# Kernel optimization log

Hardware: AMD Instinct MI355X
Metric: run time of the kernel (lower is better)

Reference implementation:

```python
import jax, jax.numpy as jnp
import numpy as np

N, D_IN, D_OUT, N_CTRS, K = 16384, 64, 64, 512, 16


def setup_inputs() -> dict:
    key = jax.random.key(0)
    k1, k2, k3, k4 = jax.random.split(key, 4)
    x = jax.random.normal(k1, (N, D_IN), dtype=jnp.float32)
    ctrs = jax.random.normal(k2, (N_CTRS, D_IN), dtype=jnp.float32)
    Wv = jax.random.normal(k3, (N_CTRS, D_IN, D_OUT), dtype=jnp.float32) * 0.02
    Ov = jax.random.normal(k4, (N_CTRS, D_OUT), dtype=jnp.float32) * 0.02
    return {"x": x, "ctrs": ctrs, "Wv": Wv, "Ov": Ov, "k": K}


def reference(x, ctrs, Wv, Ov, k):
    n = x.shape[0]
    # squared distances via expansion (same math as sum((x-c)^2), avoids [n,C,d] blowup)
    x2 = jnp.sum(x * x, axis=1, keepdims=True)            # [n,1]
    c2 = jnp.sum(ctrs * ctrs, axis=1)                     # [C]
    dist_sq = x2 + c2[None, :] - 2.0 * (x @ ctrs.T)       # [n,C]
    # k nearest centers; softmax over negative squared distances of the k selected
    neg_top, idx = jax.lax.top_k(-dist_sq, k)             # [n,k] each
    scores = jax.nn.softmax(neg_top, axis=1)              # [n,k]
    # dense soft-assignment matrix (only k nonzeros per row), as in the torch code
    A = jnp.zeros_like(dist_sq).at[jnp.arange(n)[:, None], idx].set(scores)  # [n,C]
    # per-token affine mix: sum_c A[n,c] * (x[n] @ Wv[c] + Ov[c])
    scored_weights = jnp.einsum('nc,cgp->ngp', A, Wv)     # [n,d_in,d_out]
    out = jnp.einsum('ngp,ng->np', scored_weights, x) + A @ Ov  # [n,d_out]
    return out
```

## Files before the change

### kernel.cpp

```cpp
#include <hip/hip_runtime.h>

#define N_TOK 16384
#define D 64
#define NC 512
#define KSEL 16
#define NPAIR (N_TOK * KSEL)
#define PADCAP 327168

typedef __attribute__((ext_vector_type(8))) short short8;
typedef __attribute__((ext_vector_type(16))) float float16;

__device__ __forceinline__ unsigned fkey(float f) {
    unsigned u = __float_as_uint(f);
    return (u & 0x80000000u) ? ~u : (u | 0x80000000u);
}
__device__ __forceinline__ float funkey(unsigned k) {
    unsigned u = (k & 0x80000000u) ? (k & 0x7fffffffu) : ~k;
    return __uint_as_float(u);
}
__device__ __forceinline__ unsigned short bfr(float f) {
    unsigned u = __float_as_uint(f);
    return (unsigned short)((u + 0x7FFFu + ((u >> 16) & 1u)) >> 16);
}

__device__ __forceinline__ void ins16(unsigned (&run)[16], unsigned k) {
    #pragma unroll
    for (int r = 0; r < 16; ++r) {
        unsigned mx = run[r] > k ? run[r] : k;
        unsigned mn = run[r] > k ? k : run[r];
        run[r] = mx; k = mn;
    }
}

__global__ __launch_bounds__(256) void topk12_kernel(
    const float* __restrict__ x, const float* __restrict__ ctrs,
    unsigned* __restrict__ pk) {
    __shared__ __align__(16) unsigned char pool[65536];
    float* xsT = (float*)pool;
    float* csT = (float*)(pool + 32768);
    unsigned* Sbk = (unsigned*)pool;
    unsigned* mbp = (unsigned*)pool;

    const int t = threadIdx.x;
    const int tb = blockIdx.x >> 2;
    const int p = blockIdx.x & 3;
    const int base = tb * 128;
    const int cbase = p * 128;

    #pragma unroll
    for (int i = 0; i < 8; ++i) {
        int e = t + 256 * i;
        int r = e >> 4, j = e & 15;
        int col = 64 * ((r >> 2) & 1) + 4 * (r >> 3) + (r & 3);
        float4 v = *(const float4*)(x + (base + r) * D + 4 * j);
        xsT[(4 * j + 0) * 128 + col] = v.x;
        xsT[(4 * j + 1) * 128 + col] = v.y;
        xsT[(4 * j + 2) * 128 + col] = v.z;
        xsT[(4 * j + 3) * 128 + col] = v.w;
    }
    #pragma unroll
    for (int i = 0; i < 8; ++i) {
        int e = t + 256 * i;
        int r = e >> 4, j = e & 15;
        int col = 64 * ((r >> 2) & 1) + 4 * (r >> 3) + (r & 3);
        float4 v = *(const float4*)(ctrs + (cbase + r) * D + 4 * j);
        csT[(4 * j + 0) * 128 + col] = v.x;
        csT[(4 * j + 1) * 128 + col] = v.y;
        csT[(4 * j + 2) * 128 + col] = v.z;
        csT[(4 * j + 3) * 128 + col] = v.w;
    }
    __syncthreads();

    const int tg = t >> 4;
    const int cg = t & 15;

    float acc[8][8];
    float acc2[8];
    #pragma unroll
    for (int i = 0; i < 8; ++i) {
        acc2[i] = 0.f;
        #pragma unroll
        for (int j = 0; j < 8; ++j) acc[i][j] = 0.f;
    }

    #pragma unroll 2
    for (int k = 0; k < 64; ++k) {
        const float* xr = xsT + k * 128;
        const float* cr = csT + k * 128;
        float4 xa0 = *(const float4*)(xr + 4 * tg);
        float4 xa1 = *(const float4*)(xr + 64 + 4 * tg);
        float4 cb0 = *(const float4*)(cr + 4 * cg);
        float4 cb1 = *(const float4*)(cr + 64 + 4 * cg);
        float xv[8] = {xa0.x, xa0.y, xa0.z, xa0.w, xa1.x, xa1.y, xa1.z, xa1.w};
        float cv[8] = {cb0.x, cb0.y, cb0.z, cb0.w, cb1.x, cb1.y, cb1.z, cb1.w};
        #pragma unroll
        for (int i = 0; i < 8; ++i) {
            #pragma unroll
            for (int j = 0; j < 8; ++j)
                acc[i][j] = fmaf(xv[i], cv[j], acc[i][j]);
        }
        #pragma unroll
        for (int j = 0; j < 8; ++j) acc2[j] = fmaf(cv[j], cv[j], acc2[j]);
    }
    __syncthreads();

    #pragma unroll
    for (int s = 0; s < 16; ++s) {
        const int i = s >> 1;
        const int jv = s & 1;
        unsigned kq[4];
        #pragma unroll
        for (int q = 0; q < 4; ++q) {
            int j = 4 * jv + q;
            float sq = fmaf(2.f, acc[i][j], -acc2[j]);
            kq[q] = (fkey(sq) & 0xFFFFFE00u) | (unsigned)(cbase + 8 * cg + j);
        }
        *(uint4*)(Sbk + (8 * tg + i) * 128 + 8 * cg + 4 * jv) =
            make_uint4(kq[0], kq[1], kq[2], kq[3]);
    }
    __syncthreads();

    const int tok = t & 127;
    const int h = t >> 7;
    unsigned run[16];
    #pragma unroll
    for (int r = 0; r < 16; ++r) run[r] = 0u;
    #pragma unroll
    for (int s = 0; s < 16; ++s) {
        int cq = h * 16 + ((s + tok) & 15);
        uint4 kv = *(const uint4*)(Sbk + tok * 128 + 4 * cq);
        ins16(run, kv.x); ins16(run, kv.y); ins16(run, kv.z); ins16(run, kv.w);
    }
    __syncthreads();

    #pragma unroll
    for (int r = 0; r < 16; ++r) mbp[tok * 33 + h * 16 + r] = run[r];
    __syncthreads();

    if (t < 128) {
        const unsigned* A = mbp + t * 33;
        const unsigned* B = A + 16;
        unsigned m[16];
        int ia = 0, ib = 0;
        unsigned va = A[0], vb = B[0];
        #pragma unroll
        for (int r = 0; r < 16; ++r) {
            bool ta = va > vb;
            m[r] = ta ? va : vb;
            if (ta) { ++ia; va = (ia < 16) ? A[ia] : 0u; }
            else    { ++ib; vb = (ib < 16) ? B[ib] : 0u; }
        }
        uint4* dst = (uint4*)(pk + (size_t)(base + t) * 64 + p * 16);
        dst[0] = make_uint4(m[0], m[1], m[2], m[3]);
        dst[1] = make_uint4(m[4], m[5], m[6], m[7]);
        dst[2] = make_uint4(m[8], m[9], m[10], m[11]);
        dst[3] = make_uint4(m[12], m[13], m[14], m[15]);
    }
}

__global__ __launch_bounds__(256) void topmerge_kernel(
    const unsigned* __restrict__ pk, float* __restrict__ scores,
    int* __restrict__ sidx, int* __restrict__ hist) {
    __shared__ int lhist[NC];
    const int t = threadIdx.x;
    lhist[t] = 0; lhist[t + 256] = 0;
    __syncthreads();
    const int n = blockIdx.x * 256 + t;
    const unsigned* p = pk + (size_t)n * 64;
    unsigned h[4]; int pos[4];
    #pragma unroll
    for (int w = 0; w < 4; ++w) { pos[w] = 0; h[w] = p[w * 16]; }
    float vals[16]; int ids[16];
    #pragma unroll
    for (int r = 0; r < KSEL; ++r) {
        unsigned m = h[0];
        #pragma unroll
        for (int w = 1; w < 4; ++w) m = m > h[w] ? m : h[w];
        vals[r] = funkey(m);
        ids[r] = (int)(m & 511u);
        #pragma unroll
        for (int w = 0; w < 4; ++w) {
            if (h[w] == m) {
                ++pos[w];
                h[w] = (pos[w] < KSEL) ? p[w * 16 + pos[w]] : 0u;
            }
        }
    }
    float mx = vals[0];
    float e[16]; float sum = 0.f;
    #pragma unroll
    for (int r = 0; r < KSEL; ++r) { e[r] = __expf(vals[r] - mx); sum += e[r]; }
    float inv = 1.f / sum;
    #pragma unroll
    for (int q = 0; q < 4; ++q) {
        *(float4*)(scores + n * KSEL + 4 * q) =
            make_float4(e[4*q] * inv, e[4*q+1] * inv, e[4*q+2] * inv, e[4*q+3] * inv);
        *(int4*)(sidx + n * KSEL + 4 * q) =
            make_int4(ids[4*q], ids[4*q+1], ids[4*q+2], ids[4*q+3]);
    }
    #pragma unroll
    for (int r = 0; r < KSEL; ++r) atomicAdd(&lhist[ids[r]], 1);
    __syncthreads();
    { int hv = lhist[t]; if (hv) atomicAdd(&hist[t], hv); }
    { int hv = lhist[t + 256]; if (hv) atomicAdd(&hist[t + 256], hv); }
}

__global__ __launch_bounds__(512) void scan2_kernel(const int* __restrict__ hist,
                                                    int* __restrict__ cursor,
                                                    int* __restrict__ meta) {
    __shared__ int buf[2][NC];
    int t = threadIdx.x;
    int pad = (hist[t] + 127) & ~127;
    buf[0][t] = pad;
    __syncthreads();
    int a = 0;
    for (int d = 1; d < NC; d <<= 1) {
        int val = buf[a][t] + (t >= d ? buf[a][t - d] : 0);
        buf[1 - a][t] = val;
        __syncthreads();
        a = 1 - a;
    }
    int incl = buf[a][t];
    cursor[t] = incl - pad;
    if (t == NC - 1) meta[0] = incl;
}

__global__ __launch_bounds__(256) void scatter4_kernel(
    const int* __restrict__ sidx, const float* __restrict__ scores,
    int* __restrict__ cursor, int* __restrict__ tokentab,
    float* __restrict__ scotab) {
    __shared__ int lh[NC];
    __shared__ int lbase[NC];
    const int t = threadIdx.x;
    for (int i = t; i < NC; i += 256) lh[i] = 0;
    __syncthreads();
    const int base_e = blockIdx.x * 1024;
    int myc[4];
    #pragma unroll
    for (int i = 0; i < 4; ++i) {
        int c = sidx[base_e + t + 256 * i];
        myc[i] = c;
        atomicAdd(&lh[c], 1);
    }
    __syncthreads();
    for (int i = t; i < NC; i += 256) {
        int h = lh[i];
        lbase[i] = h ? atomicAdd(&cursor[i], h) : 0;
        lh[i] = 0;
    }
    __syncthreads();
    #pragma unroll
    for (int i = 0; i < 4; ++i) {
        int e = base_e + t + 256 * i;
        int c = myc[i];
        int pos = lbase[c] + atomicAdd(&lh[c], 1);
        tokentab[pos] = (c << 19) | e;
        scotab[pos] = scores[e];
    }
}

__global__ __launch_bounds__(256) void mix15_kernel(
    const float* __restrict__ x, const float* __restrict__ Wv,
    const float* __restrict__ Ov, const int* __restrict__ tokentab,
    const float* __restrict__ scotab, const int* __restrict__ meta,
    float* __restrict__ partial) {
    __shared__ __align__(16) unsigned short Wt[64 * 72];
    __shared__ int eT[128];
    __shared__ float sT[128];

    const int t = threadIdx.x;
    const int base = blockIdx.x * 128;
    if (base >= meta[0]) return;

    const int c = (int)(((unsigned)tokentab[base]) >> 19);

    {
        const float* Wp = Wv + c * (D * D) + (t & 63);
        const int gb = (t >> 6) * 16;
        #pragma unroll
        for (int g = 0; g < 16; g += 2) {
            float v0 = Wp[(gb + g) * 64];
            float v1 = Wp[(gb + g + 1) * 64];
            unsigned pk2 = (unsigned)bfr(v0) | ((unsigned)bfr(v1) << 16);
            *(unsigned*)&Wt[(t & 63) * 72 + gb + g] = pk2;
        }
    }
    if (t < 128) {
        unsigned w = (unsigned)tokentab[base + t];
        eT[t] = (int)(w & 0x7FFFFu);
        sT[t] = scotab[base + t];
    }
    __syncthreads();

    const int lane = t & 63;
    const int wv = t >> 6;
    const int mrow = lane & 31;
    const int half = lane >> 5;
    const int row = wv * 32 + mrow;

    const int   mye = eT[row];
    const int   myn = (mye < NPAIR) ? (mye >> 4) : 0;
    const float mys = sT[row];

    const float* xp = x + myn * D + half * 8;
    float4 f[8];
    #pragma unroll
    for (int kt = 0; kt < 4; ++kt) {
        f[2 * kt]     = *(const float4*)(xp + kt * 16);
        f[2 * kt + 1] = *(const float4*)(xp + kt * 16 + 4);
    }
    short8 a[4];
    #pragma unroll
    for (int kt = 0; kt < 4; ++kt) {
        float4 u = f[2 * kt], v = f[2 * kt + 1];
        a[kt][0] = (short)bfr(u.x * mys); a[kt][1] = (short)bfr(u.y * mys);
        a[kt][2] = (short)bfr(u.z * mys); a[kt][3] = (short)bfr(u.w * mys);
        a[kt][4] = (short)bfr(v.x * mys); a[kt][5] = (short)bfr(v.y * mys);
        a[kt][6] = (short)bfr(v.z * mys); a[kt][7] = (short)bfr(v.w * mys);
    }

    float16 acc0 = {0.f,0.f,0.f,0.f,0.f,0.f,0.f,0.f,0.f,0.f,0.f,0.f,0.f,0.f,0.f,0.f};
    float16 acc1 = {0.f,0.f,0.f,0.f,0.f,0.f,0.f,0.f,0.f,0.f,0.f,0.f,0.f,0.f,0.f,0.f};

    const unsigned short* B0 = Wt + mrow * 72;
    const unsigned short* B1 = Wt + (mrow + 32) * 72;
    #pragma unroll
    for (int kt = 0; kt < 4; ++kt) {
        short8 b0 = *(const short8*)(B0 + kt * 16 + half * 8);
        short8 b1 = *(const short8*)(B1 + kt * 16 + half * 8);
        acc0 = __builtin_amdgcn_mfma_f32_32x32x16_bf16(a[kt], b0, acc0, 0, 0, 0);
        acc1 = __builtin_amdgcn_mfma_f32_32x32x16_bf16(a[kt], b1, acc1, 0, 0, 0);
    }

    const float ov0 = Ov[c * D + mrow];
    const float ov1 = Ov[c * D + 32 + mrow];
    #pragma unroll
    for (int reg = 0; reg < 16; ++reg) {
        int orow = wv * 32 + (reg & 3) + 8 * (reg >> 2) + 4 * half;
        float s = sT[orow];
        int e = eT[orow];
        if (e < NPAIR) {
            float* dst = partial + (size_t)e * D;
            dst[mrow]      = acc0[reg] + s * ov0;
            dst[32 + mrow] = acc1[reg] + s * ov1;
        }
    }
}

__global__ __launch_bounds__(256) void redu_kernel(
    const float* __restrict__ partial, float* __restrict__ out) {
    const int g = blockIdx.x * 256 + threadIdx.x;
    const int n = g >> 4;
    const int d4 = (g & 15) * 4;
    const float* p = partial + (size_t)n * (KSEL * D) + d4;
    float4 s = make_float4(0.f, 0.f, 0.f, 0.f);
    #pragma unroll
    for (int r = 0; r < KSEL; ++r) {
        float4 v = *(const float4*)(p + r * D);
        s.x += v.x; s.y += v.y; s.z += v.z; s.w += v.w;
    }
    *(float4*)(out + n * D + d4) = s;
}

__global__ __launch_bounds__(256) void mix14_kernel(
    const float* __restrict__ x, const float* __restrict__ Wv,
    const float* __restrict__ Ov, const int* __restrict__ tokentab,
    const float* __restrict__ scotab, const int* __restrict__ meta,
    float* __restrict__ out) {
    __shared__ __align__(16) unsigned short Wt[64 * 72];
    __shared__ int tT[128];
    __shared__ float sT[128];

    const int t = threadIdx.x;
    const int base = blockIdx.x * 128;
    if (base >= meta[0]) return;

    const int c = (int)(((unsigned)tokentab[base]) >> 19);

    {
        const float* Wp = Wv + c * (D * D) + (t & 63);
        const int gb = (t >> 6) * 16;
        #pragma unroll
        for (int g = 0; g < 16; g += 2) {
            float v0 = Wp[(gb + g) * 64];
            float v1 = Wp[(gb + g + 1) * 64];
            unsigned pk2 = (unsigned)bfr(v0) | ((unsigned)bfr(v1) << 16);
            *(unsigned*)&Wt[(t & 63) * 72 + gb + g] = pk2;
        }
    }
    if (t < 128) {
        unsigned w = (unsigned)tokentab[base + t];
        tT[t] = (int)((w & 0x7FFFFu) >> 4);
        sT[t] = scotab[base + t];
    }
    __syncthreads();

    const int lane = t & 63;
    const int wv = t >> 6;
    const int mrow = lane & 31;
    const int half = lane >> 5;
    const int row = wv * 32 + mrow;

    const int   myn = tT[row];
    const float mys = sT[row];

    const float* xp = x + myn * D + half * 8;
    float4 f[8];
    #pragma unroll
    for (int kt = 0; kt < 4; ++kt) {
        f[2 * kt]     = *(const float4*)(xp + kt * 16);
        f[2 * kt + 1] = *(const float4*)(xp + kt * 16 + 4);
    }
    short8 a[4];
    #pragma unroll
    for (int kt = 0; kt < 4; ++kt) {
        float4 u = f[2 * kt], v = f[2 * kt + 1];
        a[kt][0] = (short)bfr(u.x * mys); a[kt][1] = (short)bfr(u.y * mys);
        a[kt][2] = (short)bfr(u.z * mys); a[kt][3] = (short)bfr(u.w * mys);
        a[kt][4] = (short)bfr(v.x * mys); a[kt][5] = (short)bfr(v.y * mys);
        a[kt][6] = (short)bfr(v.z * mys); a[kt][7] = (short)bfr(v.w * mys);
    }

    float16 acc0 = {0.f,0.f,0.f,0.f,0.f,0.f,0.f,0.f,0.f,0.f,0.f,0.f,0.f,0.f,0.f,0.f};
    float16 acc1 = {0.f,0.f,0.f,0.f,0.f,0.f,0.f,0.f,0.f,0.f,0.f,0.f,0.f,0.f,0.f,0.f};

    const unsigned short* B0 = Wt + mrow * 72;
    const unsigned short* B1 = Wt + (mrow + 32) * 72;
    #pragma unroll
    for (int kt = 0; kt < 4; ++kt) {
        short8 b0 = *(const short8*)(B0 + kt * 16 + half * 8);
        short8 b1 = *(const short8*)(B1 + kt * 16 + half * 8);
        acc0 = __builtin_amdgcn_mfma_f32_32x32x16_bf16(a[kt], b0, acc0, 0, 0, 0);
        acc1 = __builtin_amdgcn_mfma_f32_32x32x16_bf16(a[kt], b1, acc1, 0, 0, 0);
    }

    const float ov0 = Ov[c * D + mrow];
    const float ov1 = Ov[c * D + 32 + mrow];
    #pragma unroll
    for (int reg = 0; reg < 16; ++reg) {
        int orow = wv * 32 + (reg & 3) + 8 * (reg >> 2) + 4 * half;
        float s = sT[orow];
        if (s != 0.f) {
            int n = tT[orow];
            unsafeAtomicAdd(out + n * D + mrow,      acc0[reg] + s * ov0);
            unsafeAtomicAdd(out + n * D + 32 + mrow, acc1[reg] + s * ov1);
        }
    }
}

extern "C" void kernel_launch(void* const* d_in, const int* in_sizes, int n_in,
                              void* d_out, int out_size, void* d_ws, size_t ws_size,
                              hipStream_t stream) {
    const float* x    = (const float*)d_in[0];
    const float* ctrs = (const float*)d_in[1];
    const float* Wv   = (const float*)d_in[2];
    const float* Ov   = (const float*)d_in[3];
    float* out = (float*)d_out;

    int*   hist     = (int*)d_ws + 512;
    int*   meta     = (int*)d_ws + 1024;
    int*   cursor   = (int*)d_ws + 2048;
    float* scores   = (float*)d_ws + 2560;
    int*   sidx     = (int*)d_ws + 2560 + NPAIR;
    int*   tokentab = (int*)d_ws + 2560 + 2 * NPAIR;
    float* scotab   = (float*)d_ws + 2560 + 2 * NPAIR + PADCAP;
    float* partial  = (float*)d_ws + 2560 + 2 * NPAIR + 2 * PADCAP;
    unsigned* pkbuf = (unsigned*)partial;

    const size_t need = ((size_t)2560 + 2 * (size_t)NPAIR + 2 * (size_t)PADCAP) * 4
                      + (size_t)NPAIR * D * 4;
    const bool fast = ws_size >= need;

    hipMemsetAsync(hist, 0, NC * sizeof(int), stream);
    hipMemsetAsync(scotab, 0, (size_t)PADCAP * sizeof(float), stream);
    if (fast) {
        hipMemsetAsync(tokentab, 0xFF, (size_t)PADCAP * sizeof(int), stream);
    } else {
        hipMemsetAsync(out, 0, (size_t)N_TOK * D * sizeof(float), stream);
        hipMemsetAsync(tokentab, 0, (size_t)PADCAP * sizeof(int), stream);
    }
    hipLaunchKernelGGL(topk12_kernel, dim3((N_TOK / 128) * 4), dim3(256), 0, stream,
                       x, ctrs, pkbuf);
    hipLaunchKernelGGL(topmerge_kernel, dim3(N_TOK / 256), dim3(256), 0, stream,
                       pkbuf, scores, sidx, hist);
    hipLaunchKernelGGL(scan2_kernel, dim3(1), dim3(512), 0, stream, hist, cursor, meta);
    hipLaunchKernelGGL(scatter4_kernel, dim3(256), dim3(256), 0, stream,
                       sidx, scores, cursor, tokentab, scotab);
    if (fast) {
        hipLaunchKernelGGL(mix15_kernel, dim3(PADCAP / 128), dim3(256), 0, stream,
                           x, Wv, Ov, tokentab, scotab, meta, partial);
        hipLaunchKernelGGL(redu_kernel, dim3(NPAIR / 256), dim3(256), 0, stream,
                           partial, out);
    } else {
        hipLaunchKernelGGL(mix14_kernel, dim3(PADCAP / 128), dim3(256), 0, stream,
                           x, Wv, Ov, tokentab, scotab, meta, out);
    }
}
```

Measured before the change: 166.7 us.

## Compute top-k distance GEMM with split-bf16 MFMA instead of FP32 FMA

Replaces the scalar FP32 outer-product distance computation in the top-k kernel with MFMA 32x32x16 bf16 instructions. Both x and centers are split into hi and lo bf16 parts, and three products (hi*hi, lo*hi, hi*lo) are accumulated to keep near-FP32 accuracy. Shared memory drops from 64KB to about 35KB, with a launch bound of 3 blocks per CU to raise occupancy. The candidate sort now runs in two halves of 64 centers each. The risk is that small precision differences flip near-tie top-k selections.

Result: faster. 153.3 us (-8.0%).

```diff
diff --git a/kernel.cpp b/kernel.cpp
--- a/kernel.cpp
+++ b/kernel.cpp
@@ -22,6 +22,12 @@
     unsigned u = __float_as_uint(f);
     return (unsigned short)((u + 0x7FFFu + ((u >> 16) & 1u)) >> 16);
 }
+__device__ __forceinline__ float b2f(unsigned short h) {
+    return __uint_as_float((unsigned)h << 16);
+}
+__device__ __forceinline__ unsigned pk2(unsigned short a, unsigned short b) {
+    return (unsigned)a | ((unsigned)b << 16);
+}
 
 __device__ __forceinline__ void ins16(unsigned (&run)[16], unsigned k) {
     #pragma unroll
@@ -32,103 +38,135 @@
     }
 }
 
-__global__ __launch_bounds__(256) void topk12_kernel(
+__global__ __launch_bounds__(256, 3) void topk13_kernel(
     const float* __restrict__ x, const float* __restrict__ ctrs,
     unsigned* __restrict__ pk) {
-    __shared__ __align__(16) unsigned char pool[65536];
-    float* xsT = (float*)pool;
-    float* csT = (float*)(pool + 32768);
+    __shared__ __align__(16) unsigned char pool[35328];
+    unsigned short* Cbf = (unsigned short*)pool;
     unsigned* Sbk = (unsigned*)pool;
     unsigned* mbp = (unsigned*)pool;
+    float* c2s = (float*)(pool + 34816);
 
     const int t = threadIdx.x;
+    const int lane = t & 63;
+    const int wv = t >> 6;
+    const int mrow = lane & 31;
+    const int half = lane >> 5;
     const int tb = blockIdx.x >> 2;
     const int p = blockIdx.x & 3;
     const int base = tb * 128;
     const int cbase = p * 128;
 
-    #pragma unroll
-    for (int i = 0; i < 8; ++i) {
-        int e = t + 256 * i;
-        int r = e >> 4, j = e & 15;
-        int col = 64 * ((r >> 2) & 1) + 4 * (r >> 3) + (r & 3);
-        float4 v = *(const float4*)(x + (base + r) * D + 4 * j);
-        xsT[(4 * j + 0) * 128 + col] = v.x;
-        xsT[(4 * j + 1) * 128 + col] = v.y;
-        xsT[(4 * j + 2) * 128 + col] = v.z;
-        xsT[(4 * j + 3) * 128 + col] = v.w;
-    }
-    #pragma unroll
-    for (int i = 0; i < 8; ++i) {
-        int e = t + 256 * i;
-        int r = e >> 4, j = e & 15;
-        int col = 64 * ((r >> 2) & 1) + 4 * (r >> 3) + (r & 3);
-        float4 v = *(const float4*)(ctrs + (cbase + r) * D + 4 * j);
-        csT[(4 * j + 0) * 128 + col] = v.x;
-        csT[(4 * j + 1) * 128 + col] = v.y;
-        csT[(4 * j + 2) * 128 + col] = v.z;
-        csT[(4 * j + 3) * 128 + col] = v.w;
-    }
-    __syncthreads();
-
-    const int tg = t >> 4;
-    const int cg = t & 15;
-
-    float acc[8][8];
-    float acc2[8];
-    #pragma unroll
-    for (int i = 0; i < 8; ++i) {
-        acc2[i] = 0.f;
-        #pragma unroll
-        for (int j = 0; j < 8; ++j) acc[i][j] = 0.f;
-    }
-
-    #pragma unroll 2
-    for (int k = 0; k < 64; ++k) {
-        const float* xr = xsT + k * 128;
-        const float* cr = csT + k * 128;
-        float4 xa0 = *(const float4*)(xr + 4 * tg);
-        float4 xa1 = *(const float4*)(xr + 64 + 4 * tg);
-        float4 cb0 = *(const float4*)(cr + 4 * cg);
-        float4 cb1 = *(const float4*)(cr + 64 + 4 * cg);
-        float xv[8] = {xa0.x, xa0.y, xa0.z, xa0.w, xa1.x, xa1.y, xa1.z, xa1.w};
-        float cv[8] = {cb0.x, cb0.y, cb0.z, cb0.w, cb1.x, cb1.y, cb1.z, cb1.w};
+    {
+        const int r = t >> 1, q = t & 1;
+        const float4* cp = (const float4*)(ctrs + (cbase + r) * D + q * 32);
+        unsigned short* Ch = Cbf + r * 136 + q * 32;
+        float s2 = 0.f;
         #pragma unroll
         for (int i = 0; i < 8; ++i) {
+            float4 v = cp[i];
+            s2 += v.x * v.x + v.y * v.y + v.z * v.z + v.w * v.w;
+            unsigned short h0 = bfr(v.x), h1 = bfr(v.y), h2 = bfr(v.z), h3 = bfr(v.w);
+            unsigned short l0 = bfr(v.x - b2f(h0)), l1 = bfr(v.y - b2f(h1));
+            unsigned short l2 = bfr(v.z - b2f(h2)), l3 = bfr(v.w - b2f(h3));
+            *(uint2*)(Ch + 4 * i)      = make_uint2(pk2(h0, h1), pk2(h2, h3));
+            *(uint2*)(Ch + 64 + 4 * i) = make_uint2(pk2(l0, l1), pk2(l2, l3));
+        }
+        s2 += __shfl_xor(s2, 1);
+        c2s[r] = s2;
+    }
+
+    short8 ah[4], al[4];
+    {
+        const float* xp = x + (base + wv * 32 + mrow) * D + half * 8;
+        #pragma unroll
+        for (int kt = 0; kt < 4; ++kt) {
+            float4 u = *(const float4*)(xp + kt * 16);
+            float4 v = *(const float4*)(xp + kt * 16 + 4);
+            float c[8] = {u.x, u.y, u.z, u.w, v.x, v.y, v.z, v.w};
             #pragma unroll
-            for (int j = 0; j < 8; ++j)
-                acc[i][j] = fmaf(xv[i], cv[j], acc[i][j]);
-        }
-        #pragma unroll
-        for (int j = 0; j < 8; ++j) acc2[j] = fmaf(cv[j], cv[j], acc2[j]);
-    }
-    __syncthreads();
-
-    #pragma unroll
-    for (int s = 0; s < 16; ++s) {
-        const int i = s >> 1;
-        const int jv = s & 1;
-        unsigned kq[4];
-        #pragma unroll
-        for (int q = 0; q < 4; ++q) {
-            int j = 4 * jv + q;
-            float sq = fmaf(2.f, acc[i][j], -acc2[j]);
-            kq[q] = (fkey(sq) & 0xFFFFFE00u) | (unsigned)(cbase + 8 * cg + j);
-        }
-        *(uint4*)(Sbk + (8 * tg + i) * 128 + 8 * cg + 4 * jv) =
-            make_uint4(kq[0], kq[1], kq[2], kq[3]);
-    }
-    __syncthreads();
+            for (int j = 0; j < 8; ++j) {
+                unsigned short h = bfr(c[j]);
+                ah[kt][j] = (short)h;
+                al[kt][j] = (short)bfr(c[j] - b2f(h));
+            }
+        }
+    }
+    __syncthreads();
+
+    float16 acc0 = {0.f,0.f,0.f,0.f,0.f,0.f,0.f,0.f,0.f,0.f,0.f,0.f,0.f,0.f,0.f,0.f};
+    float16 acc1 = acc0, acc2 = acc0, acc3 = acc0;
+
+    const unsigned short* Bbase = Cbf + mrow * 136 + half * 8;
+    #pragma unroll
+    for (int kt = 0; kt < 4; ++kt) {
+        const unsigned short* Bp = Bbase + kt * 16;
+        short8 b0 = *(const short8*)(Bp);
+        short8 b1 = *(const short8*)(Bp + 32 * 136);
+        short8 b2 = *(const short8*)(Bp + 64 * 136);
+        short8 b3 = *(const short8*)(Bp + 96 * 136);
+        acc0 = __builtin_amdgcn_mfma_f32_32x32x16_bf16(ah[kt], b0, acc0, 0, 0, 0);
+        acc1 = __builtin_amdgcn_mfma_f32_32x32x16_bf16(ah[kt], b1, acc1, 0, 0, 0);
+        acc2 = __builtin_amdgcn_mfma_f32_32x32x16_bf16(ah[kt], b2, acc2, 0, 0, 0);
+        acc3 = __builtin_amdgcn_mfma_f32_32x32x16_bf16(ah[kt], b3, acc3, 0, 0, 0);
+        acc0 = __builtin_amdgcn_mfma_f32_32x32x16_bf16(al[kt], b0, acc0, 0, 0, 0);
+        acc1 = __builtin_amdgcn_mfma_f32_32x32x16_bf16(al[kt], b1, acc1, 0, 0, 0);
+        acc2 = __builtin_amdgcn_mfma_f32_32x32x16_bf16(al[kt], b2, acc2, 0, 0, 0);
+        acc3 = __builtin_amdgcn_mfma_f32_32x32x16_bf16(al[kt], b3, acc3, 0, 0, 0);
+        b0 = *(const short8*)(Bp + 64);
+        b1 = *(const short8*)(Bp + 64 + 32 * 136);
+        b2 = *(const short8*)(Bp + 64 + 64 * 136);
+        b3 = *(const short8*)(Bp + 64 + 96 * 136);
+        acc0 = __builtin_amdgcn_mfma_f32_32x32x16_bf16(ah[kt], b0, acc0, 0, 0, 0);
+        acc1 = __builtin_amdgcn_mfma_f32_32x32x16_bf16(ah[kt], b1, acc1, 0, 0, 0);
+        acc2 = __builtin_amdgcn_mfma_f32_32x32x16_bf16(ah[kt], b2, acc2, 0, 0, 0);
+        acc3 = __builtin_amdgcn_mfma_f32_32x32x16_bf16(ah[kt], b3, acc3, 0, 0, 0);
+    }
+    __syncthreads();
+
+    unsigned run[16];
+    #pragma unroll
+    for (int r = 0; r < 16; ++r) run[r] = 0u;
 
     const int tok = t & 127;
     const int h = t >> 7;
-    unsigned run[16];
-    #pragma unroll
-    for (int r = 0; r < 16; ++r) run[r] = 0u;
-    #pragma unroll
-    for (int s = 0; s < 16; ++s) {
-        int cq = h * 16 + ((s + tok) & 15);
-        uint4 kv = *(const uint4*)(Sbk + tok * 128 + 4 * cq);
+
+    {
+        float ca = c2s[mrow];
+        float cb = c2s[32 + mrow];
+        #pragma unroll
+        for (int reg = 0; reg < 16; ++reg) {
+            int tokrow = wv * 32 + (reg & 3) + 8 * (reg >> 2) + 4 * half;
+            float sa = fmaf(2.f, acc0[reg], -ca);
+            float sb = fmaf(2.f, acc1[reg], -cb);
+            Sbk[tokrow * 68 + mrow]      = (fkey(sa) & 0xFFFFFE00u) | (unsigned)(cbase + mrow);
+            Sbk[tokrow * 68 + 32 + mrow] = (fkey(sb) & 0xFFFFFE00u) | (unsigned)(cbase + 32 + mrow);
+        }
+    }
+    __syncthreads();
+    #pragma unroll
+    for (int i = 0; i < 8; ++i) {
+        uint4 kv = *(const uint4*)(Sbk + tok * 68 + h * 32 + 4 * ((i + tok) & 7));
+        ins16(run, kv.x); ins16(run, kv.y); ins16(run, kv.z); ins16(run, kv.w);
+    }
+    __syncthreads();
+
+    {
+        float ca = c2s[64 + mrow];
+        float cb = c2s[96 + mrow];
+        #pragma unroll
+        for (int reg = 0; reg < 16; ++reg) {
+            int tokrow = wv * 32 + (reg & 3) + 8 * (reg >> 2) + 4 * half;
+            float sa = fmaf(2.f, acc2[reg], -ca);
+            float sb = fmaf(2.f, acc3[reg], -cb);
+            Sbk[tokrow * 68 + mrow]      = (fkey(sa) & 0xFFFFFE00u) | (unsigned)(cbase + 64 + mrow);
+            Sbk[tokrow * 68 + 32 + mrow] = (fkey(sb) & 0xFFFFFE00u) | (unsigned)(cbase + 96 + mrow);
+        }
+    }
+    __syncthreads();
+    #pragma unroll
+    for (int i = 0; i < 8; ++i) {
+        uint4 kv = *(const uint4*)(Sbk + tok * 68 + h * 32 + 4 * ((i + tok) & 7));
         ins16(run, kv.x); ins16(run, kv.y); ins16(run, kv.z); ins16(run, kv.w);
     }
     __syncthreads();
@@ -281,8 +319,8 @@
         for (int g = 0; g < 16; g += 2) {
             float v0 = Wp[(gb + g) * 64];
             float v1 = Wp[(gb + g + 1) * 64];
-            unsigned pk2 = (unsigned)bfr(v0) | ((unsigned)bfr(v1) << 16);
-            *(unsigned*)&Wt[(t & 63) * 72 + gb + g] = pk2;
+            unsigned pkw = (unsigned)bfr(v0) | ((unsigned)bfr(v1) << 16);
+            *(unsigned*)&Wt[(t & 63) * 72 + gb + g] = pkw;
         }
     }
     if (t < 128) {
@@ -384,8 +422,8 @@
         for (int g = 0; g < 16; g += 2) {
             float v0 = Wp[(gb + g) * 64];
             float v1 = Wp[(gb + g + 1) * 64];
-            unsigned pk2 = (unsigned)bfr(v0) | ((unsigned)bfr(v1) << 16);
-            *(unsigned*)&Wt[(t & 63) * 72 + gb + g] = pk2;
+            unsigned pkw = (unsigned)bfr(v0) | ((unsigned)bfr(v1) << 16);
+            *(unsigned*)&Wt[(t & 63) * 72 + gb + g] = pkw;
         }
     }
     if (t < 128) {
@@ -479,7 +517,7 @@
         hipMemsetAsync(out, 0, (size_t)N_TOK * D * sizeof(float), stream);
         hipMemsetAsync(tokentab, 0, (size_t)PADCAP * sizeof(int), stream);
     }
-    hipLaunchKernelGGL(topk12_kernel, dim3((N_TOK / 128) * 4), dim3(256), 0, stream,
+    hipLaunchKernelGGL(topk13_kernel, dim3((N_TOK / 128) * 4), dim3(256), 0, stream,
                        x, ctrs, pkbuf);
     hipLaunchKernelGGL(topmerge_kernel, dim3(N_TOK / 256), dim3(256), 0, stream,
                        pkbuf, scores, sidx, hist);
```
